# Optimization experiments

Hardware: AMD Instinct MI355X
Metric: run time of the kernel (lower is better)

Reference implementation:

```python
import jax, jax.numpy as jnp
import numpy as np

B, S, H = 2, 2048, 2048
N_HEADS = 16
HEAD_DIM = H // N_HEADS  # 128


def apply_rotary(x, cos, sin):
    # x: (B, n_heads, S, head_dim); cos/sin: (S, head_dim//2)
    d = x.shape[-1] // 2
    x1, x2 = x[..., :d], x[..., d:]
    c = cos[None, None, :x.shape[2]]
    s = sin[None, None, :x.shape[2]]
    return jnp.concatenate([x1 * c - x2 * s, x2 * c + x1 * s], axis=-1)


def setup_inputs() -> dict:
    key = jax.random.key(0)
    k1, k2, k3 = jax.random.split(key, 3)
    x = jax.random.normal(k1, (B, S, H), dtype=jnp.float32)
    qkv_w = jax.random.normal(k2, (3 * H, H), dtype=jnp.float32) * (1.0 / np.sqrt(H))
    o_w = jax.random.normal(k3, (H, H), dtype=jnp.float32) * (1.0 / np.sqrt(H))
    # rotary tables, half head_dim
    inv_freq = 1.0 / (10000.0 ** (jnp.arange(0, HEAD_DIM // 2, dtype=jnp.float32) / (HEAD_DIM // 2)))
    t = jnp.arange(S, dtype=jnp.float32)
    freqs = jnp.outer(t, inv_freq)  # (S, head_dim//2)
    cos, sin = jnp.cos(freqs), jnp.sin(freqs)
    # True = masked (strictly upper triangular)
    causal_mask = jnp.triu(jnp.ones((S, S), dtype=bool), k=1)
    return {"x": x, "qkv_w": qkv_w, "o_w": o_w, "cos": cos, "sin": sin,
            "causal_mask": causal_mask}


def reference(x, qkv_w, o_w, cos, sin, causal_mask):
    Bx, Sx, Hx = x.shape
    qkv = jnp.einsum('bsh,oh->bso', x, qkv_w)  # (B,S,3H)
    qkv = qkv.reshape(Bx, Sx, 3, N_HEADS, HEAD_DIM)
    q, k, v = qkv[:, :, 0], qkv[:, :, 1], qkv[:, :, 2]
    q = jnp.transpose(q, (0, 2, 1, 3))  # (B,nh,S,hd)
    k = jnp.transpose(k, (0, 2, 1, 3))
    v = jnp.transpose(v, (0, 2, 1, 3))
    q = apply_rotary(q, cos, sin)
    k = apply_rotary(k, cos, sin)
    scale = 1.0 / jnp.sqrt(jnp.asarray(HEAD_DIM, dtype=x.dtype))
    attn = jnp.einsum('bnqd,bnkd->bnqk', q, k) * scale
    attn = jnp.where(causal_mask[None, None], -jnp.inf, attn)
    attn = jax.nn.softmax(attn, axis=-1)
    out = jnp.einsum('bnqk,bnkd->bnqd', attn, v)
    out = jnp.transpose(out, (0, 2, 1, 3)).reshape(Bx, Sx, Hx)
    return jnp.einsum('bsh,oh->bso', out, o_w)
```

## Files before the change

kernel.cpp:

```cpp
#include <hip/hip_runtime.h>
#include <hip/hip_bf16.h>
#include <stdint.h>

typedef __attribute__((ext_vector_type(4))) float f32x4;
typedef __attribute__((ext_vector_type(8))) short s16x8;
typedef __attribute__((ext_vector_type(4))) short s16x4;

#define SWZ(g, row) ((((g) & ~7) | (((g) ^ ((row) & 7)) & 7)))

__device__ __forceinline__ unsigned short f2bf(float f) {
  unsigned u = __builtin_bit_cast(unsigned, f);
  u += 0x7fffu + ((u >> 16) & 1u);
  return (unsigned short)(u >> 16);
}

__device__ __forceinline__ void gld16(const void* g, void* l) {
  __builtin_amdgcn_global_load_lds(
      (const __attribute__((address_space(1))) void*)g,
      (__attribute__((address_space(3))) void*)l, 16, 0, 0);
}

__global__ void cvt_all(const float* __restrict__ x, const float* __restrict__ qkvw,
                        const float* __restrict__ ow, unsigned short* __restrict__ X16,
                        unsigned short* __restrict__ W16, unsigned short* __restrict__ OW16) {
  int i = blockIdx.x * blockDim.x + threadIdx.x;
  const float* src; unsigned short* dst; int off;
  if (i < 2097152)      { src = x;    dst = X16;  off = i; }
  else if (i < 5242880) { src = qkvw; dst = W16;  off = i - 2097152; }
  else                  { src = ow;   dst = OW16; off = i - 5242880; }
  float4 v = ((const float4*)src)[off];
  s16x4 o;
  o[0] = (short)f2bf(v.x); o[1] = (short)f2bf(v.y);
  o[2] = (short)f2bf(v.z); o[3] = (short)f2bf(v.w);
  ((s16x4*)dst)[off] = o;
}

#define PH_PRE \
  __builtin_amdgcn_s_barrier(); \
  asm volatile("s_waitcnt lgkmcnt(0)" ::: "memory"); \
  __builtin_amdgcn_sched_barrier(0); \
  __builtin_amdgcn_s_setprio(1);

#define PH_POST_N \
  __builtin_amdgcn_s_setprio(0); \
  __builtin_amdgcn_s_barrier();

#define PH_POST_W0 \
  __builtin_amdgcn_s_setprio(0); \
  asm volatile("s_waitcnt vmcnt(0)" ::: "memory"); \
  __builtin_amdgcn_s_barrier();

#define PH_POST_W2 \
  __builtin_amdgcn_s_setprio(0); \
  asm volatile("s_waitcnt vmcnt(2)" ::: "memory"); \
  __builtin_amdgcn_s_barrier();

#define PH_POST_W3 \
  __builtin_amdgcn_s_setprio(0); \
  asm volatile("s_waitcnt vmcnt(3)" ::: "memory"); \
  __builtin_amdgcn_s_barrier();

#define RDA(KS) \
  _Pragma("unroll") for (int j = 0; j < 4; ++j) { \
    const int ra = wm * 64 + j * 16 + lg; \
    av[j] = *(const s16x8*)(sA + ra * 128 + (SWZ(4 * (KS) + hg, ra) << 4)); }

#define STG_A(DST, ORG, KT) \
  _Pragma("unroll") for (int rr = 0; rr < 2; ++rr) { \
    const int G = rr * 512 + tid; const int row = G >> 3, g = G & 7; \
    gld16((const char*)((ORG) + (size_t)row * 2048 + (size_t)(KT) * 64) + (SWZ(g, row) << 4), \
          (DST) + rr * 8192 + tid * 16); }

#define STG_B2(DST, ORG, KT, R0) \
  _Pragma("unroll") for (int rr = (R0); rr < (R0) + 2; ++rr) { \
    const int G = rr * 512 + tid; const int row = G >> 3, g = G & 7; \
    gld16((const char*)((ORG) + (size_t)row * 2048 + (size_t)(KT) * 64) + (SWZ(g, row) << 4), \
          (DST) + rr * 8192 + tid * 16); }

#define RDB(KS, CH) \
  _Pragma("unroll") for (int b = 0; b < 3; ++b) { \
    const int bb = (CH) * 3 + b; \
    const int cb = (bb >> 1) * 128 + wn * 16 + (bb & 1) * 64 + lg; \
    bv[b] = *(const s16x8*)(sB + cb * 128 + (SWZ(4 * (KS) + hg, cb) << 4)); }

#define MM12(CH) \
  _Pragma("unroll") for (int j = 0; j < 4; ++j) \
    _Pragma("unroll") for (int b = 0; b < 3; ++b) \
      acc[j][(CH) * 3 + b] = __builtin_amdgcn_mfma_f32_16x16x32_bf16( \
          av[j], bv[b], acc[j][(CH) * 3 + b], 0, 0, 0);

__global__ __launch_bounds__(512, 1) void gemm_qkv_384(
    const unsigned short* __restrict__ A,
    const unsigned short* __restrict__ Bt,
    const float* __restrict__ cosT, const float* __restrict__ sinT,
    unsigned short* __restrict__ qOut, unsigned short* __restrict__ kOut,
    unsigned short* __restrict__ vtOut)
{
  __shared__ char smem[131072];
  const int tid = (int)threadIdx.x;
  const int wid = tid >> 6, l = tid & 63;
  const int lg = l & 15, hg = l >> 4;
  const int wm = wid >> 2, wn = wid & 3;
  const int s = ((int)blockIdx.x & 7) * 64 + ((int)blockIdx.x >> 3);
  const int bm0 = (s & 31) * 128, bn0 = (s >> 5) * 384;

  const unsigned short* Aorg = A + (size_t)bm0 * 2048;
  const unsigned short* Borg = Bt + (size_t)bn0 * 2048;

  f32x4 acc[4][6] = {};

  STG_A(smem + 0, Aorg, 0)
  STG_B2(smem + 16384, Borg, 0, 0)
  STG_B2(smem + 16384, Borg, 0, 2)
  STG_B2(smem + 16384, Borg, 0, 4)
  asm volatile("s_waitcnt vmcnt(3)" ::: "memory");
  __builtin_amdgcn_s_barrier();

  for (int t = 0; t < 31; ++t) {
    const char* sA = smem + (t & 1) * 65536;
    const char* sB = sA + 16384;
    char* dA = smem + ((t & 1) ^ 1) * 65536;
    char* dB = dA + 16384;
    s16x8 av[4], bv[3];
    RDA(0) RDB(0, 0) STG_A(dA, Aorg, t + 1)      PH_PRE MM12(0) PH_POST_W2
    RDB(0, 1)        STG_B2(dB, Borg, t + 1, 0)  PH_PRE MM12(1) PH_POST_N
    RDA(1) RDB(1, 1) STG_B2(dB, Borg, t + 1, 2)  PH_PRE MM12(1) PH_POST_N
    RDB(1, 0)        STG_B2(dB, Borg, t + 1, 4)  PH_PRE MM12(0) PH_POST_W3
  }
  {
    const char* sA = smem + 65536;
    const char* sB = sA + 16384;
    s16x8 av[4], bv[3];
    RDA(0) RDB(0, 0)  PH_PRE MM12(0) PH_POST_W0
    RDB(0, 1)         PH_PRE MM12(1) PH_POST_N
    RDA(1) RDB(1, 1)  PH_PRE MM12(1) PH_POST_N
    RDB(1, 0)         PH_PRE MM12(0)
    __builtin_amdgcn_s_setprio(0);
  }

  #pragma unroll
  for (int j = 0; j < 4; ++j) {
    const int grow0 = bm0 + wm * 64 + j * 16 + hg * 4;
    const int b_ = grow0 >> 11;
    #pragma unroll
    for (int cg = 0; cg < 3; ++cg) {
      const int og = (bn0 >> 7) + cg;
      const int tt = og >> 4, h = og & 15;
      const int d = wn * 16 + lg;
      if (tt < 2) {
        unsigned short* dst = (tt == 0) ? qOut : kOut;
        #pragma unroll
        for (int r = 0; r < 4; ++r) {
          const int gr = grow0 + r;
          const int s1 = gr & 2047;
          const float x1 = acc[j][cg * 2 + 0][r];
          const float x2 = acc[j][cg * 2 + 1][r];
          const float cv = cosT[s1 * 64 + d];
          const float sv = sinT[s1 * 64 + d];
          const size_t base = (((size_t)b_ * 16 + h) * 2048 + s1) * 128;
          dst[base + d]      = f2bf(x1 * cv - x2 * sv);
          dst[base + d + 64] = f2bf(x2 * cv + x1 * sv);
        }
      } else {
        const int s0 = grow0 & 2047;
        s16x4 p1, p2;
        #pragma unroll
        for (int r = 0; r < 4; ++r) {
          p1[r] = (short)f2bf(acc[j][cg * 2 + 0][r]);
          p2[r] = (short)f2bf(acc[j][cg * 2 + 1][r]);
        }
        *(s16x4*)(vtOut + (((size_t)b_ * 16 + h) * 128 + d)      * 2048 + s0) = p1;
        *(s16x4*)(vtOut + (((size_t)b_ * 16 + h) * 128 + d + 64) * 2048 + s0) = p2;
      }
    }
  }
}

#define RDBO(KS, CH) \
  _Pragma("unroll") for (int b = 0; b < 2; ++b) { \
    const int cb = ((CH) * 2 + b) * 64 + wn * 16 + lg; \
    bv[b] = *(const s16x8*)(sB + cb * 128 + (SWZ(4 * (KS) + hg, cb) << 4)); }

#define MMO(CH) \
  _Pragma("unroll") for (int j = 0; j < 4; ++j) \
    _Pragma("unroll") for (int b = 0; b < 2; ++b) \
      acc[j][(CH) * 2 + b] = __builtin_amdgcn_mfma_f32_16x16x32_bf16( \
          av[j], bv[b], acc[j][(CH) * 2 + b], 0, 0, 0);

__global__ __launch_bounds__(512, 1) void gemm_op_256(
    const unsigned short* __restrict__ A,
    const unsigned short* __restrict__ Bt,
    float* __restrict__ C)
{
  __shared__ char smem[98304];
  const int tid = (int)threadIdx.x;
  const int wid = tid >> 6, l = tid & 63;
  const int lg = l & 15, hg = l >> 4;
  const int wm = wid >> 2, wn = wid & 3;
  const int s = ((int)blockIdx.x & 7) * 32 + ((int)blockIdx.x >> 3);
  const int bm0 = (s & 31) * 128, bn0 = (s >> 5) * 256;

  const unsigned short* Aorg = A + (size_t)bm0 * 2048;
  const unsigned short* Borg = Bt + (size_t)bn0 * 2048;

  f32x4 acc[4][4] = {};

  STG_A(smem + 0, Aorg, 0)
  STG_B2(smem + 16384, Borg, 0, 0)
  STG_B2(smem + 16384, Borg, 0, 2)
  asm volatile("s_waitcnt vmcnt(2)" ::: "memory");
  __builtin_amdgcn_s_barrier();

  for (int t = 0; t < 31; ++t) {
    const char* sA = smem + (t & 1) * 49152;
    const char* sB = sA + 16384;
    char* dA = smem + ((t & 1) ^ 1) * 49152;
    char* dB = dA + 16384;
    s16x8 av[4], bv[2];
    RDA(0) RDBO(0, 0) STG_A(dA, Aorg, t + 1)      PH_PRE MMO(0) PH_POST_W2
    RDBO(0, 1)        STG_B2(dB, Borg, t + 1, 0)  PH_PRE MMO(1) PH_POST_N
    RDA(1) RDBO(1, 1) STG_B2(dB, Borg, t + 1, 2)  PH_PRE MMO(1) PH_POST_N
    RDBO(1, 0)                                    PH_PRE MMO(0) PH_POST_W2
  }
  {
    const char* sA = smem + 49152;
    const char* sB = sA + 16384;
    s16x8 av[4], bv[2];
    RDA(0) RDBO(0, 0)  PH_PRE MMO(0) PH_POST_W0
    RDBO(0, 1)         PH_PRE MMO(1) PH_POST_N
    RDA(1) RDBO(1, 1)  PH_PRE MMO(1) PH_POST_N
    RDBO(1, 0)         PH_PRE MMO(0)
    __builtin_amdgcn_s_setprio(0);
  }

  #pragma unroll
  for (int j = 0; j < 4; ++j) {
    const int row0 = bm0 + wm * 64 + j * 16 + hg * 4;
    #pragma unroll
    for (int b = 0; b < 4; ++b) {
      const int col = bn0 + b * 64 + wn * 16 + lg;
      #pragma unroll
      for (int r = 0; r < 4; ++r)
        C[(size_t)(row0 + r) * 2048 + col] = acc[j][b][r];
    }
  }
}

__global__ __launch_bounds__(256) void attn_fwd(
    const unsigned short* __restrict__ Qp, const unsigned short* __restrict__ Kp,
    const unsigned short* __restrict__ Vt, unsigned short* __restrict__ AO)
{
  __shared__ char sK[16384];
  __shared__ char sV[16384];
  __shared__ char sP[8192];

  const int tid = (int)threadIdx.x, w = tid >> 6, l = tid & 63;
  const int lg = l & 15, hg = l >> 4;
  const int bid = (int)blockIdx.x;
  const int p = bid >> 8, c = bid & 255;
  const int j = c >> 5, bh = c & 31;
  const int qt = (p == 0) ? j : (p == 1) ? 31 - j : (p == 2) ? 8 + j : 23 - j;
  const size_t qkBase = (size_t)bh * 2048 * 128;
  const int qw0 = qt * 64 + w * 16;
  const int qi = qw0 + lg;

  s16x8 qf[4];
  for (int ks = 0; ks < 4; ++ks)
    qf[ks] = *(const s16x8*)(Qp + qkBase + (size_t)(qw0 + lg) * 128 + ks * 32 + hg * 8);

  f32x4 acc_o[8] = {};
  float mrun = -1e30f, lrun = 0.f;
  const float SCALE = 0.08838834764831845f;
  const float L2E = 1.4426950408889634f;
  const float CS = SCALE * L2E;

  const int nkv = qt + 1;
  for (int kv = 0; kv < nkv; ++kv) {
    const int kv0 = kv * 64;
    __syncthreads();
    for (int i = 0; i < 4; ++i) {
      const int G = w * 256 + i * 64 + l;
      const int rk = G >> 4, gk = G & 15;
      gld16((const char*)(Kp + qkBase + (size_t)(kv0 + rk) * 128) + (SWZ(gk, rk) << 4),
            sK + w * 4096 + i * 1024);
      const int rv = G >> 3, gv = G & 7;
      gld16((const char*)(Vt + qkBase + (size_t)rv * 2048 + kv0) + (SWZ(gv, rv) << 4),
            sV + w * 4096 + i * 1024);
    }
    asm volatile("s_waitcnt vmcnt(0)" ::: "memory");
    __syncthreads();

    f32x4 accs[4] = {};
    for (int ks = 0; ks < 4; ++ks)
      for (int kf = 0; kf < 4; ++kf) {
        const int row = kf * 16 + lg;
        const int g = SWZ(4 * ks + hg, row);
        s16x8 kfrag = *(const s16x8*)(sK + row * 256 + (g << 4));
        accs[kf] = __builtin_amdgcn_mfma_f32_16x16x32_bf16(kfrag, qf[ks], accs[kf], 0, 0, 0);
      }

    const bool diag = (kv == qt);
    float raw[4][4];
    float mt = -1e30f;
    #pragma unroll
    for (int kf = 0; kf < 4; ++kf)
      #pragma unroll
      for (int r = 0; r < 4; ++r) {
        float s = accs[kf][r];
        if (diag) {
          const int jj = kv0 + kf * 16 + hg * 4 + r;
          s = (jj > qi) ? -1e30f : s;
        }
        raw[kf][r] = s;
        mt = fmaxf(mt, s);
      }
    mt = fmaxf(mt, __shfl_xor(mt, 16));
    mt = fmaxf(mt, __shfl_xor(mt, 32));
    mt *= SCALE;
    if (!__all(mt - mrun <= 8.0f)) {
      const float mnew = fmaxf(mrun, mt);
      const float alpha = exp2f((mrun - mnew) * L2E);
      float ar[4];
      #pragma unroll
      for (int r = 0; r < 4; ++r) ar[r] = __shfl(alpha, hg * 4 + r);
      #pragma unroll
      for (int f = 0; f < 8; ++f)
        #pragma unroll
        for (int r = 0; r < 4; ++r) acc_o[f][r] *= ar[r];
      lrun *= alpha;
      mrun = mnew;
    }
    const float mL = mrun * L2E;
    float ls = 0.f;
    char* pw = sP + w * 2048;
    #pragma unroll
    for (int kf = 0; kf < 4; ++kf) {
      s16x4 pk;
      #pragma unroll
      for (int r = 0; r < 4; ++r) {
        const float e = exp2f(raw[kf][r] * CS - mL);
        ls += e;
        pk[r] = (short)f2bf(e);
      }
      const int j0 = kf * 16 + hg * 4;
      *(s16x4*)(pw + lg * 128 + (SWZ(j0 >> 3, lg) << 4) + ((j0 * 2) & 15)) = pk;
    }
    ls += __shfl_xor(ls, 16);
    ls += __shfl_xor(ls, 32);
    lrun += ls;
    asm volatile("" ::: "memory");

    for (int jc = 0; jc < 2; ++jc) {
      const int gp = SWZ(hg + 4 * jc, lg);
      s16x8 pa = *(const s16x8*)(pw + lg * 128 + (gp << 4));
      for (int f = 0; f < 8; ++f) {
        const int rv = f * 16 + lg;
        const int gv = SWZ(hg + 4 * jc, rv);
        s16x8 vb = *(const s16x8*)(sV + rv * 128 + (gv << 4));
        acc_o[f] = __builtin_amdgcn_mfma_f32_16x16x32_bf16(pa, vb, acc_o[f], 0, 0, 0);
      }
    }
  }

  float linv[4];
  for (int r = 0; r < 4; ++r) linv[r] = 1.0f / __shfl(lrun, hg * 4 + r);
  const int b = bh >> 4, h = bh & 15;
  for (int f = 0; f < 8; ++f) {
    const int d = h * 128 + f * 16 + lg;
    for (int r = 0; r < 4; ++r) {
      const int srow = qw0 + hg * 4 + r;
      AO[((size_t)(b * 2048 + srow)) * 2048 + d] = f2bf(acc_o[f][r] * linv[r]);
    }
  }
}

extern "C" void kernel_launch(void* const* d_in, const int* in_sizes, int n_in,
                              void* d_out, int out_size, void* d_ws, size_t ws_size,
                              hipStream_t stream) {
  const float* x    = (const float*)d_in[0];
  const float* qkvw = (const float*)d_in[1];
  const float* ow   = (const float*)d_in[2];
  const float* cosT = (const float*)d_in[3];
  const float* sinT = (const float*)d_in[4];
  float* out = (float*)d_out;

  unsigned short* X16  = (unsigned short*)d_ws;
  unsigned short* W16  = X16  + (size_t)8388608;
  unsigned short* OW16 = W16  + (size_t)12582912;
  unsigned short* Qp   = OW16 + (size_t)4194304;
  unsigned short* Kp   = Qp   + (size_t)8388608;
  unsigned short* Vtp  = Kp   + (size_t)8388608;
  unsigned short* AO   = Vtp  + (size_t)8388608;

  cvt_all<<<24576, 256, 0, stream>>>(x, qkvw, ow, X16, W16, OW16);

  gemm_qkv_384<<<512, 512, 0, stream>>>(X16, W16, cosT, sinT, Qp, Kp, Vtp);

  attn_fwd<<<1024, 256, 0, stream>>>(Qp, Kp, Vtp, AO);

  gemm_op_256<<<256, 512, 0, stream>>>(AO, OW16, out);
}
```

Baseline: 234.1 us.

## Double-buffer K/V tiles and process 128-query blocks with two row-groups per wave

The attention kernel now works on 128-row query tiles, and each wave handles two 16-row query groups that share every K and V fragment read from LDS. K/V tiles are double-buffered, so the next tile's global-to-LDS load is issued while the current one is being computed. The grid is halved to 512 blocks with a simpler causal load-balancing pairing. This is meant to cut LDS traffic per MFMA and hide global load latency, at the cost of more registers and LDS per block, which may lower occupancy.

```diff
diff --git a/kernel.cpp b/kernel.cpp
--- a/kernel.cpp
+++ b/kernel.cpp
@@ -246,130 +246,172 @@
   }
 }
 
+#define ASTG(BB, KV0) \
+  _Pragma("unroll") for (int i = 0; i < 4; ++i) { \
+    const int G = w * 256 + i * 64 + l; \
+    const int rk = G >> 4, gk = G & 15; \
+    gld16((const char*)(Kp + qkBase + (size_t)((KV0) + rk) * 128) + (SWZ(gk, rk) << 4), \
+          &sK[BB][w * 4096 + i * 1024]); \
+    const int rv = G >> 3, gv = G & 7; \
+    gld16((const char*)(Vt + qkBase + (size_t)rv * 2048 + (KV0)) + (SWZ(gv, rv) << 4), \
+          &sV[BB][w * 4096 + i * 1024]); \
+  }
+
+#define SMAX(SS, MM, LL, AO, QI, PB, DG) { \
+  float mt = -1e30f; \
+  _Pragma("unroll") for (int kf = 0; kf < 4; ++kf) \
+    _Pragma("unroll") for (int r = 0; r < 4; ++r) { \
+      float sv_ = SS[kf][r]; \
+      if (DG) { \
+        const int jj = kv0 + kf * 16 + hg * 4 + r; \
+        sv_ = (jj > (QI)) ? -1e30f : sv_; \
+        SS[kf][r] = sv_; \
+      } \
+      mt = fmaxf(mt, sv_); \
+    } \
+  mt = fmaxf(mt, __shfl_xor(mt, 16)); \
+  mt = fmaxf(mt, __shfl_xor(mt, 32)); \
+  mt *= SCALE; \
+  if (!__all(mt - MM <= 8.0f)) { \
+    const float mnew = fmaxf(MM, mt); \
+    const float alpha = exp2f((MM - mnew) * L2E); \
+    float ar[4]; \
+    _Pragma("unroll") for (int r = 0; r < 4; ++r) ar[r] = __shfl(alpha, hg * 4 + r); \
+    _Pragma("unroll") for (int f = 0; f < 8; ++f) \
+      _Pragma("unroll") for (int r = 0; r < 4; ++r) AO[f][r] *= ar[r]; \
+    LL *= alpha; \
+    MM = mnew; \
+  } \
+  { const float mL = MM * L2E; \
+    float ls = 0.f; \
+    _Pragma("unroll") for (int kf = 0; kf < 4; ++kf) { \
+      s16x4 pk; \
+      _Pragma("unroll") for (int r = 0; r < 4; ++r) { \
+        const float e = exp2f(SS[kf][r] * CS - mL); \
+        ls += e; \
+        pk[r] = (short)f2bf(e); \
+      } \
+      const int j0 = kf * 16 + hg * 4; \
+      *(s16x4*)((PB) + lg * 128 + (SWZ(j0 >> 3, lg) << 4) + ((j0 * 2) & 15)) = pk; \
+    } \
+    ls += __shfl_xor(ls, 16); \
+    ls += __shfl_xor(ls, 32); \
+    LL += ls; } }
+
 __global__ __launch_bounds__(256) void attn_fwd(
     const unsigned short* __restrict__ Qp, const unsigned short* __restrict__ Kp,
     const unsigned short* __restrict__ Vt, unsigned short* __restrict__ AO)
 {
-  __shared__ char sK[16384];
-  __shared__ char sV[16384];
-  __shared__ char sP[8192];
+  __shared__ char sK[2][16384];
+  __shared__ char sV[2][16384];
+  __shared__ char sP[16384];
 
   const int tid = (int)threadIdx.x, w = tid >> 6, l = tid & 63;
   const int lg = l & 15, hg = l >> 4;
   const int bid = (int)blockIdx.x;
   const int p = bid >> 8, c = bid & 255;
   const int j = c >> 5, bh = c & 31;
-  const int qt = (p == 0) ? j : (p == 1) ? 31 - j : (p == 2) ? 8 + j : 23 - j;
+  const int qt = p ? (15 - j) : j;
   const size_t qkBase = (size_t)bh * 2048 * 128;
-  const int qw0 = qt * 64 + w * 16;
-  const int qi = qw0 + lg;
-
-  s16x8 qf[4];
-  for (int ks = 0; ks < 4; ++ks)
-    qf[ks] = *(const s16x8*)(Qp + qkBase + (size_t)(qw0 + lg) * 128 + ks * 32 + hg * 8);
-
-  f32x4 acc_o[8] = {};
-  float mrun = -1e30f, lrun = 0.f;
+  const int qw0 = qt * 128 + w * 32;
+  const int qiA = qw0 + lg, qiB = qw0 + 16 + lg;
+
+  char* const pbA = sP + w * 4096;
+  char* const pbB = pbA + 2048;
+
+  s16x8 qfA[4], qfB[4];
+  #pragma unroll
+  for (int ks = 0; ks < 4; ++ks) {
+    qfA[ks] = *(const s16x8*)(Qp + qkBase + (size_t)(qw0 + lg) * 128 + ks * 32 + hg * 8);
+    qfB[ks] = *(const s16x8*)(Qp + qkBase + (size_t)(qw0 + 16 + lg) * 128 + ks * 32 + hg * 8);
+  }
+
+  f32x4 aoA[8] = {}, aoB[8] = {};
+  float mA = -1e30f, lA = 0.f, mB = -1e30f, lB = 0.f;
   const float SCALE = 0.08838834764831845f;
   const float L2E = 1.4426950408889634f;
   const float CS = SCALE * L2E;
 
-  const int nkv = qt + 1;
+  const int nkv = 2 * qt + 2;
+
+  ASTG(0, 0)
+  ASTG(1, 64)
+  asm volatile("s_waitcnt vmcnt(8)" ::: "memory");
+  __builtin_amdgcn_s_barrier();
+
   for (int kv = 0; kv < nkv; ++kv) {
+    const int cur = kv & 1;
     const int kv0 = kv * 64;
-    __syncthreads();
-    for (int i = 0; i < 4; ++i) {
-      const int G = w * 256 + i * 64 + l;
-      const int rk = G >> 4, gk = G & 15;
-      gld16((const char*)(Kp + qkBase + (size_t)(kv0 + rk) * 128) + (SWZ(gk, rk) << 4),
-            sK + w * 4096 + i * 1024);
-      const int rv = G >> 3, gv = G & 7;
-      gld16((const char*)(Vt + qkBase + (size_t)rv * 2048 + kv0) + (SWZ(gv, rv) << 4),
-            sV + w * 4096 + i * 1024);
-    }
-    asm volatile("s_waitcnt vmcnt(0)" ::: "memory");
-    __syncthreads();
-
-    f32x4 accs[4] = {};
-    for (int ks = 0; ks < 4; ++ks)
-      for (int kf = 0; kf < 4; ++kf) {
-        const int row = kf * 16 + lg;
-        const int g = SWZ(4 * ks + hg, row);
-        s16x8 kfrag = *(const s16x8*)(sK + row * 256 + (g << 4));
-        accs[kf] = __builtin_amdgcn_mfma_f32_16x16x32_bf16(kfrag, qf[ks], accs[kf], 0, 0, 0);
+    const char* cK = sK[cur];
+    const char* cV = sV[cur];
+    const bool actB = (kv0 <= qw0 + 31);
+    const bool actA = (kv0 <= qw0 + 15);
+
+    if (actB) {
+      f32x4 sSA[4] = {}, sSB[4] = {};
+      #pragma unroll
+      for (int ks = 0; ks < 4; ++ks)
+        #pragma unroll
+        for (int kf = 0; kf < 4; ++kf) {
+          const int row = kf * 16 + lg;
+          s16x8 kfrag = *(const s16x8*)(cK + row * 256 + (SWZ(4 * ks + hg, row) << 4));
+          sSB[kf] = __builtin_amdgcn_mfma_f32_16x16x32_bf16(kfrag, qfB[ks], sSB[kf], 0, 0, 0);
+          if (actA)
+            sSA[kf] = __builtin_amdgcn_mfma_f32_16x16x32_bf16(kfrag, qfA[ks], sSA[kf], 0, 0, 0);
+        }
+
+      const bool dgB = (kv0 + 63 > qw0 + 16);
+      SMAX(sSB, mB, lB, aoB, qiB, pbB, dgB)
+      if (actA) {
+        const bool dgA = (kv0 + 63 > qw0);
+        SMAX(sSA, mA, lA, aoA, qiA, pbA, dgA)
       }
-
-    const bool diag = (kv == qt);
-    float raw[4][4];
-    float mt = -1e30f;
-    #pragma unroll
-    for (int kf = 0; kf < 4; ++kf)
+      asm volatile("" ::: "memory");
+
       #pragma unroll
-      for (int r = 0; r < 4; ++r) {
-        float s = accs[kf][r];
-        if (diag) {
-          const int jj = kv0 + kf * 16 + hg * 4 + r;
-          s = (jj > qi) ? -1e30f : s;
+      for (int jc = 0; jc < 2; ++jc) {
+        const int gp = SWZ(hg + 4 * jc, lg);
+        s16x8 paB = *(const s16x8*)(pbB + lg * 128 + (gp << 4));
+        s16x8 paA;
+        if (actA) paA = *(const s16x8*)(pbA + lg * 128 + (gp << 4));
+        #pragma unroll
+        for (int f = 0; f < 8; ++f) {
+          const int rv = f * 16 + lg;
+          s16x8 vb = *(const s16x8*)(cV + rv * 128 + (SWZ(hg + 4 * jc, rv) << 4));
+          aoB[f] = __builtin_amdgcn_mfma_f32_16x16x32_bf16(paB, vb, aoB[f], 0, 0, 0);
+          if (actA)
+            aoA[f] = __builtin_amdgcn_mfma_f32_16x16x32_bf16(paA, vb, aoA[f], 0, 0, 0);
         }
-        raw[kf][r] = s;
-        mt = fmaxf(mt, s);
-      }
-    mt = fmaxf(mt, __shfl_xor(mt, 16));
-    mt = fmaxf(mt, __shfl_xor(mt, 32));
-    mt *= SCALE;
-    if (!__all(mt - mrun <= 8.0f)) {
-      const float mnew = fmaxf(mrun, mt);
-      const float alpha = exp2f((mrun - mnew) * L2E);
-      float ar[4];
-      #pragma unroll
-      for (int r = 0; r < 4; ++r) ar[r] = __shfl(alpha, hg * 4 + r);
-      #pragma unroll
-      for (int f = 0; f < 8; ++f)
-        #pragma unroll
-        for (int r = 0; r < 4; ++r) acc_o[f][r] *= ar[r];
-      lrun *= alpha;
-      mrun = mnew;
-    }
-    const float mL = mrun * L2E;
-    float ls = 0.f;
-    char* pw = sP + w * 2048;
-    #pragma unroll
-    for (int kf = 0; kf < 4; ++kf) {
-      s16x4 pk;
-      #pragma unroll
-      for (int r = 0; r < 4; ++r) {
-        const float e = exp2f(raw[kf][r] * CS - mL);
-        ls += e;
-        pk[r] = (short)f2bf(e);
-      }
-      const int j0 = kf * 16 + hg * 4;
-      *(s16x4*)(pw + lg * 128 + (SWZ(j0 >> 3, lg) << 4) + ((j0 * 2) & 15)) = pk;
-    }
-    ls += __shfl_xor(ls, 16);
-    ls += __shfl_xor(ls, 32);
-    lrun += ls;
-    asm volatile("" ::: "memory");
-
-    for (int jc = 0; jc < 2; ++jc) {
-      const int gp = SWZ(hg + 4 * jc, lg);
-      s16x8 pa = *(const s16x8*)(pw + lg * 128 + (gp << 4));
-      for (int f = 0; f < 8; ++f) {
-        const int rv = f * 16 + lg;
-        const int gv = SWZ(hg + 4 * jc, rv);
-        s16x8 vb = *(const s16x8*)(sV + rv * 128 + (gv << 4));
-        acc_o[f] = __builtin_amdgcn_mfma_f32_16x16x32_bf16(pa, vb, acc_o[f], 0, 0, 0);
       }
     }
-  }
-
-  float linv[4];
-  for (int r = 0; r < 4; ++r) linv[r] = 1.0f / __shfl(lrun, hg * 4 + r);
+
+    asm volatile("s_waitcnt lgkmcnt(0)" ::: "memory");
+    __builtin_amdgcn_s_barrier();
+    if (kv + 2 < nkv) {
+      ASTG(cur, kv0 + 128)
+      asm volatile("s_waitcnt vmcnt(8)" ::: "memory");
+    } else {
+      asm volatile("s_waitcnt vmcnt(0)" ::: "memory");
+    }
+    __builtin_amdgcn_s_barrier();
+  }
+
   const int b = bh >> 4, h = bh & 15;
+  float liA[4], liB[4];
+  #pragma unroll
+  for (int r = 0; r < 4; ++r) {
+    liA[r] = 1.0f / __shfl(lA, hg * 4 + r);
+    liB[r] = 1.0f / __shfl(lB, hg * 4 + r);
+  }
+  #pragma unroll
   for (int f = 0; f < 8; ++f) {
     const int d = h * 128 + f * 16 + lg;
+    #pragma unroll
     for (int r = 0; r < 4; ++r) {
-      const int srow = qw0 + hg * 4 + r;
-      AO[((size_t)(b * 2048 + srow)) * 2048 + d] = f2bf(acc_o[f][r] * linv[r]);
+      const int srA = qw0 + hg * 4 + r;
+      const int srB = qw0 + 16 + hg * 4 + r;
+      AO[((size_t)(b * 2048 + srA)) * 2048 + d] = f2bf(aoA[f][r] * liA[r]);
+      AO[((size_t)(b * 2048 + srB)) * 2048 + d] = f2bf(aoB[f][r] * liB[r]);
     }
   }
 }
@@ -396,7 +438,7 @@
 
   gemm_qkv_384<<<512, 512, 0, stream>>>(X16, W16, cosT, sinT, Qp, Kp, Vtp);
 
-  attn_fwd<<<1024, 256, 0, stream>>>(Qp, Kp, Vtp, AO);
+  attn_fwd<<<512, 256, 0, stream>>>(Qp, Kp, Vtp, AO);
 
   gemm_op_256<<<256, 512, 0, stream>>>(AO, OW16, out);
 }
```

New measurement: 403.9 us. 1.72x slower.

## Double-buffer K/V loads, switch attention to 32x32 MFMA with 128-row query tiles

Applied to the files above, without the earlier changes.

The attention kernel now prefetches the next K/V tile into a second LDS buffer while computing on the current one, so global loads overlap compute instead of running in a serial load/wait/compute loop. Each block handles 128 query rows (32 per wave) using 32x32x16 bf16 MFMAs, which halves the grid and doubles K/V reuse per load. Causal work is skipped per wave for KV tiles beyond its rows, and the block-to-tile mapping is changed for load balance. In exchange LDS use roughly doubles and register pressure rises, which can cut occupancy, and the grid has fewer blocks.

```diff
diff --git a/kernel.cpp b/kernel.cpp
--- a/kernel.cpp
+++ b/kernel.cpp
@@ -3,10 +3,12 @@
 #include <stdint.h>
 
 typedef __attribute__((ext_vector_type(4))) float f32x4;
+typedef __attribute__((ext_vector_type(16))) float f32x16;
 typedef __attribute__((ext_vector_type(8))) short s16x8;
 typedef __attribute__((ext_vector_type(4))) short s16x4;
 
 #define SWZ(g, row) ((((g) & ~7) | (((g) ^ ((row) & 7)) & 7)))
+#define SWZ4(g, row) ((g) ^ ((row) & 15))
 
 __device__ __forceinline__ unsigned short f2bf(float f) {
   unsigned u = __builtin_bit_cast(unsigned, f);
@@ -246,130 +248,154 @@
   }
 }
 
+#define ASTG(BB, KV0) \
+  _Pragma("unroll") for (int i = 0; i < 4; ++i) { \
+    const int G = w * 256 + i * 64 + l; \
+    const int rk = G >> 4, gk = G & 15; \
+    gld16((const char*)(Kp + qkBase + (size_t)((KV0) + rk) * 128) + (SWZ4(gk, rk) << 4), \
+          &sK[BB][w * 4096 + i * 1024]); \
+    const int rv = G >> 3, gv = G & 7; \
+    gld16((const char*)(Vt + qkBase + (size_t)rv * 2048 + (KV0)) + (SWZ(gv, rv) << 4), \
+          &sV[BB][w * 4096 + i * 1024]); \
+  }
+
 __global__ __launch_bounds__(256) void attn_fwd(
     const unsigned short* __restrict__ Qp, const unsigned short* __restrict__ Kp,
     const unsigned short* __restrict__ Vt, unsigned short* __restrict__ AO)
 {
-  __shared__ char sK[16384];
-  __shared__ char sV[16384];
-  __shared__ char sP[8192];
+  __shared__ char sK[2][16384];
+  __shared__ char sV[2][16384];
+  __shared__ char sP[16384];
 
   const int tid = (int)threadIdx.x, w = tid >> 6, l = tid & 63;
-  const int lg = l & 15, hg = l >> 4;
+  const int ql = l & 31, hg2 = l >> 5;
   const int bid = (int)blockIdx.x;
   const int p = bid >> 8, c = bid & 255;
   const int j = c >> 5, bh = c & 31;
-  const int qt = (p == 0) ? j : (p == 1) ? 31 - j : (p == 2) ? 8 + j : 23 - j;
+  const int qt = p ? (15 - j) : j;
   const size_t qkBase = (size_t)bh * 2048 * 128;
-  const int qw0 = qt * 64 + w * 16;
-  const int qi = qw0 + lg;
-
-  s16x8 qf[4];
-  for (int ks = 0; ks < 4; ++ks)
-    qf[ks] = *(const s16x8*)(Qp + qkBase + (size_t)(qw0 + lg) * 128 + ks * 32 + hg * 8);
-
-  f32x4 acc_o[8] = {};
+  const int qw0 = qt * 128 + w * 32;
+  const int qi = qw0 + ql;
+  char* const pw = sP + w * 4096;
+
+  s16x8 qf[8];
+  #pragma unroll
+  for (int ks = 0; ks < 8; ++ks)
+    qf[ks] = *(const s16x8*)(Qp + qkBase + (size_t)(qw0 + ql) * 128 + ks * 16 + hg2 * 8);
+
+  f32x16 ao[4] = {};
   float mrun = -1e30f, lrun = 0.f;
   const float SCALE = 0.08838834764831845f;
   const float L2E = 1.4426950408889634f;
   const float CS = SCALE * L2E;
 
-  const int nkv = qt + 1;
+  const int nkv = 2 * qt + 2;
+
+  ASTG(0, 0)
+  ASTG(1, 64)
+  asm volatile("s_waitcnt vmcnt(8)" ::: "memory");
+  __builtin_amdgcn_s_barrier();
+
   for (int kv = 0; kv < nkv; ++kv) {
+    const int cur = kv & 1;
     const int kv0 = kv * 64;
-    __syncthreads();
-    for (int i = 0; i < 4; ++i) {
-      const int G = w * 256 + i * 64 + l;
-      const int rk = G >> 4, gk = G & 15;
-      gld16((const char*)(Kp + qkBase + (size_t)(kv0 + rk) * 128) + (SWZ(gk, rk) << 4),
-            sK + w * 4096 + i * 1024);
-      const int rv = G >> 3, gv = G & 7;
-      gld16((const char*)(Vt + qkBase + (size_t)rv * 2048 + kv0) + (SWZ(gv, rv) << 4),
-            sV + w * 4096 + i * 1024);
+    const char* cK = sK[cur];
+    const char* cV = sV[cur];
+    const bool act = (kv0 <= qw0 + 31);
+
+    if (act) {
+      f32x16 sS0 = {}, sS1 = {};
+      #pragma unroll
+      for (int ks = 0; ks < 8; ++ks) {
+        s16x8 k0 = *(const s16x8*)(cK + ql * 256 + (SWZ4(2 * ks + hg2, ql) << 4));
+        s16x8 k1 = *(const s16x8*)(cK + (32 + ql) * 256 + (SWZ4(2 * ks + hg2, 32 + ql) << 4));
+        sS0 = __builtin_amdgcn_mfma_f32_32x32x16_bf16(k0, qf[ks], sS0, 0, 0, 0);
+        sS1 = __builtin_amdgcn_mfma_f32_32x32x16_bf16(k1, qf[ks], sS1, 0, 0, 0);
+      }
+
+      const bool dg = (kv0 + 63 > qw0);
+      if (dg) {
+        #pragma unroll
+        for (int r = 0; r < 16; ++r) {
+          const int jl = (r & 3) + 8 * (r >> 2) + 4 * hg2;
+          if (kv0 + jl > qi)      sS0[r] = -1e30f;
+          if (kv0 + 32 + jl > qi) sS1[r] = -1e30f;
+        }
+      }
+      float mt = -1e30f;
+      #pragma unroll
+      for (int r = 0; r < 16; ++r) {
+        mt = fmaxf(mt, sS0[r]);
+        mt = fmaxf(mt, sS1[r]);
+      }
+      mt = fmaxf(mt, __shfl_xor(mt, 32));
+      mt *= SCALE;
+      if (!__all(mt - mrun <= 8.0f)) {
+        const float mnew = fmaxf(mrun, mt);
+        const float alpha = exp2f((mrun - mnew) * L2E);
+        #pragma unroll
+        for (int r = 0; r < 16; ++r) {
+          const float ar = __shfl(alpha, (r & 3) + 8 * (r >> 2) + 4 * hg2);
+          ao[0][r] *= ar; ao[1][r] *= ar; ao[2][r] *= ar; ao[3][r] *= ar;
+        }
+        lrun *= alpha;
+        mrun = mnew;
+      }
+      const float mL = mrun * L2E;
+      float ls = 0.f;
+      #pragma unroll
+      for (int rq = 0; rq < 4; ++rq) {
+        s16x4 pk0, pk1;
+        #pragma unroll
+        for (int i = 0; i < 4; ++i) {
+          const float e0 = exp2f(sS0[rq * 4 + i] * CS - mL); ls += e0; pk0[i] = (short)f2bf(e0);
+          const float e1 = exp2f(sS1[rq * 4 + i] * CS - mL); ls += e1; pk1[i] = (short)f2bf(e1);
+        }
+        *(s16x4*)(pw + ql * 128 + (SWZ(rq, ql) << 4) + hg2 * 8) = pk0;
+        *(s16x4*)(pw + ql * 128 + (SWZ(4 + rq, ql) << 4) + hg2 * 8) = pk1;
+      }
+      ls += __shfl_xor(ls, 32);
+      lrun += ls;
+      asm volatile("" ::: "memory");
+
+      s16x8 pf[4];
+      #pragma unroll
+      for (int ks2 = 0; ks2 < 4; ++ks2)
+        pf[ks2] = *(const s16x8*)(pw + ql * 128 + (SWZ(2 * ks2 + hg2, ql) << 4));
+      #pragma unroll
+      for (int db = 0; db < 4; ++db) {
+        const int vr = db * 32 + ql;
+        #pragma unroll
+        for (int ks2 = 0; ks2 < 4; ++ks2) {
+          s16x8 vf = *(const s16x8*)(cV + vr * 128 + (SWZ(2 * ks2 + hg2, vr) << 4));
+          ao[db] = __builtin_amdgcn_mfma_f32_32x32x16_bf16(pf[ks2], vf, ao[db], 0, 0, 0);
+        }
+      }
     }
-    asm volatile("s_waitcnt vmcnt(0)" ::: "memory");
-    __syncthreads();
-
-    f32x4 accs[4] = {};
-    for (int ks = 0; ks < 4; ++ks)
-      for (int kf = 0; kf < 4; ++kf) {
-        const int row = kf * 16 + lg;
-        const int g = SWZ(4 * ks + hg, row);
-        s16x8 kfrag = *(const s16x8*)(sK + row * 256 + (g << 4));
-        accs[kf] = __builtin_amdgcn_mfma_f32_16x16x32_bf16(kfrag, qf[ks], accs[kf], 0, 0, 0);
-      }
-
-    const bool diag = (kv == qt);
-    float raw[4][4];
-    float mt = -1e30f;
+
+    asm volatile("s_waitcnt lgkmcnt(0)" ::: "memory");
+    __builtin_amdgcn_s_barrier();
+    if (kv + 2 < nkv) {
+      ASTG(cur, kv0 + 128)
+      asm volatile("s_waitcnt vmcnt(8)" ::: "memory");
+    } else {
+      asm volatile("s_waitcnt vmcnt(0)" ::: "memory");
+    }
+    __builtin_amdgcn_s_barrier();
+  }
+
+  float li[16];
+  #pragma unroll
+  for (int r = 0; r < 16; ++r)
+    li[r] = 1.0f / __shfl(lrun, (r & 3) + 8 * (r >> 2) + 4 * hg2);
+  const int b = bh >> 4, h = bh & 15;
+  #pragma unroll
+  for (int db = 0; db < 4; ++db) {
+    const int d = h * 128 + db * 32 + ql;
     #pragma unroll
-    for (int kf = 0; kf < 4; ++kf)
-      #pragma unroll
-      for (int r = 0; r < 4; ++r) {
-        float s = accs[kf][r];
-        if (diag) {
-          const int jj = kv0 + kf * 16 + hg * 4 + r;
-          s = (jj > qi) ? -1e30f : s;
-        }
-        raw[kf][r] = s;
-        mt = fmaxf(mt, s);
-      }
-    mt = fmaxf(mt, __shfl_xor(mt, 16));
-    mt = fmaxf(mt, __shfl_xor(mt, 32));
-    mt *= SCALE;
-    if (!__all(mt - mrun <= 8.0f)) {
-      const float mnew = fmaxf(mrun, mt);
-      const float alpha = exp2f((mrun - mnew) * L2E);
-      float ar[4];
-      #pragma unroll
-      for (int r = 0; r < 4; ++r) ar[r] = __shfl(alpha, hg * 4 + r);
-      #pragma unroll
-      for (int f = 0; f < 8; ++f)
-        #pragma unroll
-        for (int r = 0; r < 4; ++r) acc_o[f][r] *= ar[r];
-      lrun *= alpha;
-      mrun = mnew;
-    }
-    const float mL = mrun * L2E;
-    float ls = 0.f;
-    char* pw = sP + w * 2048;
-    #pragma unroll
-    for (int kf = 0; kf < 4; ++kf) {
-      s16x4 pk;
-      #pragma unroll
-      for (int r = 0; r < 4; ++r) {
-        const float e = exp2f(raw[kf][r] * CS - mL);
-        ls += e;
-        pk[r] = (short)f2bf(e);
-      }
-      const int j0 = kf * 16 + hg * 4;
-      *(s16x4*)(pw + lg * 128 + (SWZ(j0 >> 3, lg) << 4) + ((j0 * 2) & 15)) = pk;
-    }
-    ls += __shfl_xor(ls, 16);
-    ls += __shfl_xor(ls, 32);
-    lrun += ls;
-    asm volatile("" ::: "memory");
-
-    for (int jc = 0; jc < 2; ++jc) {
-      const int gp = SWZ(hg + 4 * jc, lg);
-      s16x8 pa = *(const s16x8*)(pw + lg * 128 + (gp << 4));
-      for (int f = 0; f < 8; ++f) {
-        const int rv = f * 16 + lg;
-        const int gv = SWZ(hg + 4 * jc, rv);
-        s16x8 vb = *(const s16x8*)(sV + rv * 128 + (gv << 4));
-        acc_o[f] = __builtin_amdgcn_mfma_f32_16x16x32_bf16(pa, vb, acc_o[f], 0, 0, 0);
-      }
-    }
-  }
-
-  float linv[4];
-  for (int r = 0; r < 4; ++r) linv[r] = 1.0f / __shfl(lrun, hg * 4 + r);
-  const int b = bh >> 4, h = bh & 15;
-  for (int f = 0; f < 8; ++f) {
-    const int d = h * 128 + f * 16 + lg;
-    for (int r = 0; r < 4; ++r) {
-      const int srow = qw0 + hg * 4 + r;
-      AO[((size_t)(b * 2048 + srow)) * 2048 + d] = f2bf(acc_o[f][r] * linv[r]);
+    for (int r = 0; r < 16; ++r) {
+      const int q = qw0 + (r & 3) + 8 * (r >> 2) + 4 * hg2;
+      AO[((size_t)(b * 2048 + q)) * 2048 + d] = f2bf(ao[db][r] * li[r]);
     }
   }
 }
@@ -396,7 +422,7 @@
 
   gemm_qkv_384<<<512, 512, 0, stream>>>(X16, W16, cosT, sinT, Qp, Kp, Vtp);
 
-  attn_fwd<<<1024, 256, 0, stream>>>(Qp, Kp, Vtp, AO);
+  attn_fwd<<<512, 256, 0, stream>>>(Qp, Kp, Vtp, AO);
 
   gemm_op_256<<<256, 512, 0, stream>>>(AO, OW16, out);
 }
```

Result: slower. 240.2 us (+2.6%).

## Retile QKV GEMM to 256x256 blocks with 384 workgroups

Applied to the files above, without the earlier changes.

The QKV projection GEMM moves from 128x384 output tiles on 512 workgroups to 256x256 tiles on 384 workgroups, with each wave now computing 128x64. The LDS staging, fragment reads and MFMA schedule are rewritten into four phases that reuse B fragments across two A halves. The RoPE and V-transpose epilogue is remapped to the new accumulator layout. This raises arithmetic intensity per tile and cuts redundant global loads, at the cost of more accumulator registers and a wave count (384) that fits the CU count less evenly.

```diff
diff --git a/kernel.cpp b/kernel.cpp
--- a/kernel.cpp
+++ b/kernel.cpp
@@ -55,41 +55,37 @@
   asm volatile("s_waitcnt vmcnt(2)" ::: "memory"); \
   __builtin_amdgcn_s_barrier();
 
-#define PH_POST_W3 \
-  __builtin_amdgcn_s_setprio(0); \
-  asm volatile("s_waitcnt vmcnt(3)" ::: "memory"); \
-  __builtin_amdgcn_s_barrier();
-
-#define RDA(KS) \
+#define STGQ_A(DA, KT, I) \
+  _Pragma("unroll") for (int rr = 0; rr < 2; ++rr) { \
+    const int L = (I) * 2 + rr; \
+    const int G = L * 512 + tid; const int row = G >> 3, g = G & 7; \
+    gld16((const char*)(Aorg + (size_t)row * 2048 + (size_t)(KT) * 64) + (SWZ(g, row) << 4), \
+          (DA) + L * 8192 + tid * 16); }
+
+#define STGQ_B(DB, KT, I) \
+  _Pragma("unroll") for (int rr = 0; rr < 2; ++rr) { \
+    const int L = (I) * 2 + rr; \
+    const int G = L * 512 + tid; const int row = G >> 3, g = G & 7; \
+    gld16((const char*)(Borg + (size_t)row * 2048 + (size_t)(KT) * 64) + (SWZ(g, row) << 4), \
+          (DB) + L * 8192 + tid * 16); }
+
+#define RDAQ(AV, J0, KS) \
   _Pragma("unroll") for (int j = 0; j < 4; ++j) { \
-    const int ra = wm * 64 + j * 16 + lg; \
-    av[j] = *(const s16x8*)(sA + ra * 128 + (SWZ(4 * (KS) + hg, ra) << 4)); }
-
-#define STG_A(DST, ORG, KT) \
-  _Pragma("unroll") for (int rr = 0; rr < 2; ++rr) { \
-    const int G = rr * 512 + tid; const int row = G >> 3, g = G & 7; \
-    gld16((const char*)((ORG) + (size_t)row * 2048 + (size_t)(KT) * 64) + (SWZ(g, row) << 4), \
-          (DST) + rr * 8192 + tid * 16); }
-
-#define STG_B2(DST, ORG, KT, R0) \
-  _Pragma("unroll") for (int rr = (R0); rr < (R0) + 2; ++rr) { \
-    const int G = rr * 512 + tid; const int row = G >> 3, g = G & 7; \
-    gld16((const char*)((ORG) + (size_t)row * 2048 + (size_t)(KT) * 64) + (SWZ(g, row) << 4), \
-          (DST) + rr * 8192 + tid * 16); }
-
-#define RDB(KS, CH) \
-  _Pragma("unroll") for (int b = 0; b < 3; ++b) { \
-    const int bb = (CH) * 3 + b; \
-    const int cb = (bb >> 1) * 128 + wn * 16 + (bb & 1) * 64 + lg; \
-    bv[b] = *(const s16x8*)(sB + cb * 128 + (SWZ(4 * (KS) + hg, cb) << 4)); }
-
-#define MM12(CH) \
+    const int ra = wm * 128 + ((J0) + j) * 16 + lg; \
+    AV[j] = *(const s16x8*)(sA + ra * 128 + (SWZ(4 * (KS) + hg, ra) << 4)); }
+
+#define RDBQ(BV, KS) \
+  _Pragma("unroll") for (int f = 0; f < 4; ++f) { \
+    const int cb = (wn >> 1) * 128 + (wn & 1) * 32 + (f & 1) * 16 + (f >> 1) * 64 + lg; \
+    BV[f] = *(const s16x8*)(sB + cb * 128 + (SWZ(4 * (KS) + hg, cb) << 4)); }
+
+#define MMQ(AV, BV, J0) \
   _Pragma("unroll") for (int j = 0; j < 4; ++j) \
-    _Pragma("unroll") for (int b = 0; b < 3; ++b) \
-      acc[j][(CH) * 3 + b] = __builtin_amdgcn_mfma_f32_16x16x32_bf16( \
-          av[j], bv[b], acc[j][(CH) * 3 + b], 0, 0, 0);
-
-__global__ __launch_bounds__(512, 1) void gemm_qkv_384(
+    _Pragma("unroll") for (int f = 0; f < 4; ++f) \
+      acc[(J0) + j][f] = __builtin_amdgcn_mfma_f32_16x16x32_bf16( \
+          AV[j], BV[f], acc[(J0) + j][f], 0, 0, 0);
+
+__global__ __launch_bounds__(512, 1) void gemm_qkv_256x(
     const unsigned short* __restrict__ A,
     const unsigned short* __restrict__ Bt,
     const float* __restrict__ cosT, const float* __restrict__ sinT,
@@ -101,73 +97,78 @@
   const int wid = tid >> 6, l = tid & 63;
   const int lg = l & 15, hg = l >> 4;
   const int wm = wid >> 2, wn = wid & 3;
-  const int s = ((int)blockIdx.x & 7) * 64 + ((int)blockIdx.x >> 3);
-  const int bm0 = (s & 31) * 128, bn0 = (s >> 5) * 384;
+  const int s = ((int)blockIdx.x & 7) * 48 + ((int)blockIdx.x >> 3);
+  const int bm0 = (s & 15) * 256, bn0 = (s >> 4) * 256;
 
   const unsigned short* Aorg = A + (size_t)bm0 * 2048;
   const unsigned short* Borg = Bt + (size_t)bn0 * 2048;
 
-  f32x4 acc[4][6] = {};
-
-  STG_A(smem + 0, Aorg, 0)
-  STG_B2(smem + 16384, Borg, 0, 0)
-  STG_B2(smem + 16384, Borg, 0, 2)
-  STG_B2(smem + 16384, Borg, 0, 4)
-  asm volatile("s_waitcnt vmcnt(3)" ::: "memory");
-  __builtin_amdgcn_s_barrier();
+  f32x4 acc[8][4] = {};
+
+  {
+    char* dA = smem;
+    char* dB = smem + 32768;
+    STGQ_A(dA, 0, 0) STGQ_A(dA, 0, 1) STGQ_B(dB, 0, 0) STGQ_B(dB, 0, 1)
+    asm volatile("s_waitcnt vmcnt(0)" ::: "memory");
+    __builtin_amdgcn_s_barrier();
+  }
 
   for (int t = 0; t < 31; ++t) {
     const char* sA = smem + (t & 1) * 65536;
-    const char* sB = sA + 16384;
+    const char* sB = sA + 32768;
     char* dA = smem + ((t & 1) ^ 1) * 65536;
-    char* dB = dA + 16384;
-    s16x8 av[4], bv[3];
-    RDA(0) RDB(0, 0) STG_A(dA, Aorg, t + 1)      PH_PRE MM12(0) PH_POST_W2
-    RDB(0, 1)        STG_B2(dB, Borg, t + 1, 0)  PH_PRE MM12(1) PH_POST_N
-    RDA(1) RDB(1, 1) STG_B2(dB, Borg, t + 1, 2)  PH_PRE MM12(1) PH_POST_N
-    RDB(1, 0)        STG_B2(dB, Borg, t + 1, 4)  PH_PRE MM12(0) PH_POST_W3
+    char* dB = dA + 32768;
+    s16x8 avlo[4], avhi[4], bv[4];
+    RDAQ(avlo, 0, 0) RDBQ(bv, 0) STGQ_A(dA, t + 1, 0)  PH_PRE MMQ(avlo, bv, 0) PH_POST_N
+    RDAQ(avhi, 4, 0)             STGQ_A(dA, t + 1, 1)  PH_PRE MMQ(avhi, bv, 4) PH_POST_N
+    RDAQ(avhi, 4, 1) RDBQ(bv, 1) STGQ_B(dB, t + 1, 0)  PH_PRE MMQ(avhi, bv, 4) PH_POST_N
+    RDAQ(avlo, 0, 1)             STGQ_B(dB, t + 1, 1)  PH_PRE MMQ(avlo, bv, 0) PH_POST_W0
   }
   {
     const char* sA = smem + 65536;
-    const char* sB = sA + 16384;
-    s16x8 av[4], bv[3];
-    RDA(0) RDB(0, 0)  PH_PRE MM12(0) PH_POST_W0
-    RDB(0, 1)         PH_PRE MM12(1) PH_POST_N
-    RDA(1) RDB(1, 1)  PH_PRE MM12(1) PH_POST_N
-    RDB(1, 0)         PH_PRE MM12(0)
+    const char* sB = sA + 32768;
+    s16x8 avlo[4], avhi[4], bv[4];
+    RDAQ(avlo, 0, 0) RDBQ(bv, 0)  PH_PRE MMQ(avlo, bv, 0) PH_POST_N
+    RDAQ(avhi, 4, 0)              PH_PRE MMQ(avhi, bv, 4) PH_POST_N
+    RDAQ(avhi, 4, 1) RDBQ(bv, 1)  PH_PRE MMQ(avhi, bv, 4) PH_POST_N
+    RDAQ(avlo, 0, 1)              PH_PRE MMQ(avlo, bv, 0)
     __builtin_amdgcn_s_setprio(0);
   }
 
+  const int og = (bn0 >> 7) + (wn >> 1);
+  const int tt = og >> 4, h = og & 15;
   #pragma unroll
-  for (int j = 0; j < 4; ++j) {
-    const int grow0 = bm0 + wm * 64 + j * 16 + hg * 4;
+  for (int j = 0; j < 8; ++j) {
+    const int grow0 = bm0 + wm * 128 + j * 16 + hg * 4;
     const int b_ = grow0 >> 11;
-    #pragma unroll
-    for (int cg = 0; cg < 3; ++cg) {
-      const int og = (bn0 >> 7) + cg;
-      const int tt = og >> 4, h = og & 15;
-      const int d = wn * 16 + lg;
-      if (tt < 2) {
-        unsigned short* dst = (tt == 0) ? qOut : kOut;
+    if (tt < 2) {
+      unsigned short* dst = (tt == 0) ? qOut : kOut;
+      #pragma unroll
+      for (int f = 0; f < 2; ++f) {
+        const int d = (wn & 1) * 32 + f * 16 + lg;
         #pragma unroll
         for (int r = 0; r < 4; ++r) {
           const int gr = grow0 + r;
           const int s1 = gr & 2047;
-          const float x1 = acc[j][cg * 2 + 0][r];
-          const float x2 = acc[j][cg * 2 + 1][r];
+          const float x1 = acc[j][f][r];
+          const float x2 = acc[j][f + 2][r];
           const float cv = cosT[s1 * 64 + d];
           const float sv = sinT[s1 * 64 + d];
           const size_t base = (((size_t)b_ * 16 + h) * 2048 + s1) * 128;
           dst[base + d]      = f2bf(x1 * cv - x2 * sv);
           dst[base + d + 64] = f2bf(x2 * cv + x1 * sv);
         }
-      } else {
-        const int s0 = grow0 & 2047;
+      }
+    } else {
+      const int s0 = grow0 & 2047;
+      #pragma unroll
+      for (int f = 0; f < 2; ++f) {
+        const int d = (wn & 1) * 32 + f * 16 + lg;
         s16x4 p1, p2;
         #pragma unroll
         for (int r = 0; r < 4; ++r) {
-          p1[r] = (short)f2bf(acc[j][cg * 2 + 0][r]);
-          p2[r] = (short)f2bf(acc[j][cg * 2 + 1][r]);
+          p1[r] = (short)f2bf(acc[j][f][r]);
+          p2[r] = (short)f2bf(acc[j][f + 2][r]);
         }
         *(s16x4*)(vtOut + (((size_t)b_ * 16 + h) * 128 + d)      * 2048 + s0) = p1;
         *(s16x4*)(vtOut + (((size_t)b_ * 16 + h) * 128 + d + 64) * 2048 + s0) = p2;
@@ -175,6 +176,23 @@
     }
   }
 }
+
+#define STG_A(DST, ORG, KT) \
+  _Pragma("unroll") for (int rr = 0; rr < 2; ++rr) { \
+    const int G = rr * 512 + tid; const int row = G >> 3, g = G & 7; \
+    gld16((const char*)((ORG) + (size_t)row * 2048 + (size_t)(KT) * 64) + (SWZ(g, row) << 4), \
+          (DST) + rr * 8192 + tid * 16); }
+
+#define STG_B2(DST, ORG, KT, R0) \
+  _Pragma("unroll") for (int rr = (R0); rr < (R0) + 2; ++rr) { \
+    const int G = rr * 512 + tid; const int row = G >> 3, g = G & 7; \
+    gld16((const char*)((ORG) + (size_t)row * 2048 + (size_t)(KT) * 64) + (SWZ(g, row) << 4), \
+          (DST) + rr * 8192 + tid * 16); }
+
+#define RDA(KS) \
+  _Pragma("unroll") for (int j = 0; j < 4; ++j) { \
+    const int ra = wm * 64 + j * 16 + lg; \
+    av[j] = *(const s16x8*)(sA + ra * 128 + (SWZ(4 * (KS) + hg, ra) << 4)); }
 
 #define RDBO(KS, CH) \
   _Pragma("unroll") for (int b = 0; b < 2; ++b) { \
@@ -394,7 +412,7 @@
 
   cvt_all<<<24576, 256, 0, stream>>>(x, qkvw, ow, X16, W16, OW16);
 
-  gemm_qkv_384<<<512, 512, 0, stream>>>(X16, W16, cosT, sinT, Qp, Kp, Vtp);
+  gemm_qkv_256x<<<384, 512, 0, stream>>>(X16, W16, cosT, sinT, Qp, Kp, Vtp);
 
   attn_fwd<<<1024, 256, 0, stream>>>(Qp, Kp, Vtp, AO);
 
```

Result: slower. 256.0 us (+9.4%).
